# Kernel optimization log

Hardware: AMD Instinct MI355X
Metric: run time of the kernel (lower is better)

## Reference

```python
import jax, jax.numpy as jnp
import numpy as np

B, H, W, C = 128, 256, 1024, 1
N_HOLES = 5
PROB = 1.0
HOLE_MINW, HOLE_MAXW = W // 10, int(W / 2.5)   # 102, 409
HOLE_MINH, HOLE_MAXH = H // 10, int(H / 2.5)   # 25, 102


def setup_inputs() -> dict:
    key = jax.random.key(0)
    k0, k1, k2, k3, k4, k5 = jax.random.split(key, 6)
    x = jax.random.normal(k0, (B, H, W, C), dtype=jnp.float32)
    # hole centers: tf.random.uniform((bsz,n), 0, dim-1, int32) -> [0, dim-1)
    xs = jax.random.randint(k1, (B, N_HOLES), 0, W - 1, dtype=jnp.int32)
    ys = jax.random.randint(k2, (B, N_HOLES), 0, H - 1, dtype=jnp.int32)
    # hole sizes: raw in [0, max-min); reference adds the min offset
    xs_w_raw = jax.random.randint(k3, (B, N_HOLES), 0, HOLE_MAXW - HOLE_MINW, dtype=jnp.int32)
    ys_h_raw = jax.random.randint(k4, (B, N_HOLES), 0, HOLE_MAXH - HOLE_MINH, dtype=jnp.int32)
    # per-hole activation uniforms (hole active iff act_rand < PROB)
    act_rand = jax.random.uniform(k5, (B, N_HOLES), dtype=jnp.float32)
    return {"x": x, "xs": xs, "ys": ys, "xs_w_raw": xs_w_raw,
            "ys_h_raw": ys_h_raw, "act_rand": act_rand}


def _build_mask(xs, ys, xs_w_raw, ys_h_raw, act_rand):
    xs_w = xs_w_raw + HOLE_MINW                      # (B, N) hole widths
    ys_h = ys_h_raw + HOLE_MINH                      # (B, N) hole heights
    xs_start = jnp.clip(xs - xs_w // 2, 0, W - 2)
    xs_end   = jnp.clip(xs + xs_w // 2, 1, W - 1)
    ys_start = jnp.clip(ys - ys_h // 2, 0, H - 2)
    ys_end   = jnp.clip(ys + ys_h // 2, 1, H - 1)
    act = act_rand < PROB                            # (B, N) hole-wise activation
    idx_h = jnp.arange(H)
    idx_w = jnp.arange(W)
    mask = jnp.zeros((B, H, W), dtype=bool)
    for n in range(N_HOLES):                         # small fixed hole count
        mh = (ys_start[:, n, None] <= idx_h) & (idx_h <= ys_end[:, n, None])  # (B, H)
        mw = (xs_start[:, n, None] <= idx_w) & (idx_w <= xs_end[:, n, None])  # (B, W)
        m = mh[:, :, None] & mw[:, None, :]                                   # (B, H, W)
        mask = mask | (m & act[:, n, None, None])
    return mask


def reference(x, xs, ys, xs_w_raw, ys_h_raw, act_rand):
    mask = _build_mask(xs, ys, xs_w_raw, ys_h_raw, act_rand)   # (B, H, W) bool
    maskf = mask[..., None].astype(x.dtype)                    # (B, H, W, 1)
    fill = jnp.mean(x)  # hole_fill='min' path: hf = ones * reduce_mean(x)
    return x * (1.0 - maskf) + maskf * fill
```

## Files before the change

### kernel.cpp

```cpp
#include <hip/hip_runtime.h>


#define BB 128
#define HH 256
#define WW 1024
#define N_HOLES 5
#define HOLE_MINW (WW / 10)
#define HOLE_MINH (HH / 10)
#define N_ELEM (BB * HH * WW)
#define RED_BLOCKS 2048

__global__ __launch_bounds__(256) void reduce_kernel(
    const float* __restrict__ x, float* __restrict__ partials) {
  int tid = blockIdx.x * blockDim.x + threadIdx.x;
  int stride = gridDim.x * blockDim.x;
  const float4* x4 = (const float4*)x;
  const int n4 = N_ELEM / 4;
  float s = 0.0f;
  for (int i = tid; i < n4; i += stride) {
    float4 v = x4[i];
    s += (v.x + v.y) + (v.z + v.w);
  }
  #pragma unroll
  for (int off = 32; off > 0; off >>= 1) s += __shfl_down(s, off, 64);
  __shared__ float wsum[4];
  int lane = threadIdx.x & 63;
  int wave = threadIdx.x >> 6;
  if (lane == 0) wsum[wave] = s;
  __syncthreads();
  if (threadIdx.x == 0)
    partials[blockIdx.x] = (wsum[0] + wsum[1]) + (wsum[2] + wsum[3]);
}

__global__ __launch_bounds__(256) void finalize_kernel(
    const float* __restrict__ partials, float* __restrict__ mean_out) {
  float s = 0.0f;
  for (int i = threadIdx.x; i < RED_BLOCKS; i += 256) s += partials[i];
  #pragma unroll
  for (int off = 32; off > 0; off >>= 1) s += __shfl_down(s, off, 64);
  __shared__ float wsum[4];
  int lane = threadIdx.x & 63;
  int wave = threadIdx.x >> 6;
  if (lane == 0) wsum[wave] = s;
  __syncthreads();
  if (threadIdx.x == 0) {
    float t = (wsum[0] + wsum[1]) + (wsum[2] + wsum[3]);
    mean_out[0] = t * (1.0f / (float)N_ELEM);
  }
}

__global__ __launch_bounds__(256) void apply_kernel(
    const float* __restrict__ x,
    const int* __restrict__ xs, const int* __restrict__ ys,
    const int* __restrict__ xs_w_raw, const int* __restrict__ ys_h_raw,
    const float* __restrict__ act_rand,
    const float* __restrict__ mean_ptr,
    float* __restrict__ out) {
  int row = blockIdx.x;
  int b = row >> 8;
  int h = row & 255;

  float mean = mean_ptr[0];

  int lo[N_HOLES], hi[N_HOLES];
  #pragma unroll
  for (int n = 0; n < N_HOLES; ++n) {
    int base = b * N_HOLES + n;
    int cx = xs[base];
    int cy = ys[base];
    int hw = (xs_w_raw[base] + HOLE_MINW) >> 1;
    int hh = (ys_h_raw[base] + HOLE_MINH) >> 1;
    int ys_s = min(max(cy - hh, 0), HH - 2);
    int ys_e = min(max(cy + hh, 1), HH - 1);
    bool act = act_rand[base] < 1.0f;
    bool in_row = act && (ys_s <= h) && (h <= ys_e);
    int xs_s = min(max(cx - hw, 0), WW - 2);
    int xs_e = min(max(cx + hw, 1), WW - 1);
    lo[n] = in_row ? xs_s : 1;
    hi[n] = in_row ? xs_e : 0;
  }

  int w0 = (int)threadIdx.x * 4;
  long idx = (long)row * WW + w0;
  float4 v = *(const float4*)(x + idx);
  float r[4] = {v.x, v.y, v.z, v.w};
  #pragma unroll
  for (int j = 0; j < 4; ++j) {
    int w = w0 + j;
    bool m = false;
    #pragma unroll
    for (int n = 0; n < N_HOLES; ++n)
      m = m || ((lo[n] <= w) && (w <= hi[n]));
    if (m) r[j] = mean;
  }
  float4 o;
  o.x = r[0]; o.y = r[1]; o.z = r[2]; o.w = r[3];
  *(float4*)(out + idx) = o;
}

extern "C" void kernel_launch(void* const* d_in, const int* in_sizes, int n_in,
                              void* d_out, int out_size, void* d_ws, size_t ws_size,
                              hipStream_t stream) {
  const float* x        = (const float*)d_in[0];
  const int* xs         = (const int*)d_in[1];
  const int* ys         = (const int*)d_in[2];
  const int* xs_w_raw   = (const int*)d_in[3];
  const int* ys_h_raw   = (const int*)d_in[4];
  const float* act_rand = (const float*)d_in[5];
  float* out = (float*)d_out;

  float* partials = (float*)d_ws;
  float* mean_ptr = partials + RED_BLOCKS;

  reduce_kernel<<<RED_BLOCKS, 256, 0, stream>>>(x, partials);
  finalize_kernel<<<1, 256, 0, stream>>>(partials, mean_ptr);
  apply_kernel<<<BB * HH, 256, 0, stream>>>(x, xs, ys, xs_w_raw, ys_h_raw,
                                            act_rand, mean_ptr, out);
}
```

Before: 269.5 us.

## Fuse copy into reduction pass and fill only hole rectangles afterward

```diff
diff --git a/kernel.cpp b/kernel.cpp
--- a/kernel.cpp
+++ b/kernel.cpp
@@ -9,16 +9,20 @@
 #define HOLE_MINH (HH / 10)
 #define N_ELEM (BB * HH * WW)
 #define RED_BLOCKS 2048
+#define ROW_SLICES 8
 
-__global__ __launch_bounds__(256) void reduce_kernel(
-    const float* __restrict__ x, float* __restrict__ partials) {
+__global__ __launch_bounds__(256) void copy_reduce_kernel(
+    const float* __restrict__ x, float* __restrict__ out,
+    float* __restrict__ partials) {
   int tid = blockIdx.x * blockDim.x + threadIdx.x;
   int stride = gridDim.x * blockDim.x;
   const float4* x4 = (const float4*)x;
+  float4* out4 = (float4*)out;
   const int n4 = N_ELEM / 4;
   float s = 0.0f;
   for (int i = tid; i < n4; i += stride) {
     float4 v = x4[i];
+    out4[i] = v;
     s += (v.x + v.y) + (v.z + v.w);
   }
   #pragma unroll
@@ -32,70 +36,52 @@
     partials[blockIdx.x] = (wsum[0] + wsum[1]) + (wsum[2] + wsum[3]);
 }
 
-__global__ __launch_bounds__(256) void finalize_kernel(
-    const float* __restrict__ partials, float* __restrict__ mean_out) {
+__global__ __launch_bounds__(256) void fill_holes_kernel(
+    const int* __restrict__ xs, const int* __restrict__ ys,
+    const int* __restrict__ xs_w_raw, const int* __restrict__ ys_h_raw,
+    const float* __restrict__ act_rand,
+    const float* __restrict__ partials,
+    float* __restrict__ out) {
   float s = 0.0f;
   for (int i = threadIdx.x; i < RED_BLOCKS; i += 256) s += partials[i];
   #pragma unroll
   for (int off = 32; off > 0; off >>= 1) s += __shfl_down(s, off, 64);
   __shared__ float wsum[4];
+  __shared__ float mean_sh;
   int lane = threadIdx.x & 63;
   int wave = threadIdx.x >> 6;
   if (lane == 0) wsum[wave] = s;
   __syncthreads();
   if (threadIdx.x == 0) {
     float t = (wsum[0] + wsum[1]) + (wsum[2] + wsum[3]);
-    mean_out[0] = t * (1.0f / (float)N_ELEM);
+    mean_sh = t * (1.0f / (float)N_ELEM);
   }
-}
+  __syncthreads();
+  float mean = mean_sh;
 
-__global__ __launch_bounds__(256) void apply_kernel(
-    const float* __restrict__ x,
-    const int* __restrict__ xs, const int* __restrict__ ys,
-    const int* __restrict__ xs_w_raw, const int* __restrict__ ys_h_raw,
-    const float* __restrict__ act_rand,
-    const float* __restrict__ mean_ptr,
-    float* __restrict__ out) {
-  int row = blockIdx.x;
-  int b = row >> 8;
-  int h = row & 255;
+  int bid = blockIdx.x;
+  int b = bid / (N_HOLES * ROW_SLICES);
+  int rem = bid % (N_HOLES * ROW_SLICES);
+  int n = rem / ROW_SLICES;
+  int slice = rem % ROW_SLICES;
 
-  float mean = mean_ptr[0];
+  int base = b * N_HOLES + n;
+  if (!(act_rand[base] < 1.0f)) return;
+  int cx = xs[base];
+  int cy = ys[base];
+  int hw = (xs_w_raw[base] + HOLE_MINW) >> 1;
+  int hh = (ys_h_raw[base] + HOLE_MINH) >> 1;
+  int ys_s = min(max(cy - hh, 0), HH - 2);
+  int ys_e = min(max(cy + hh, 1), HH - 1);
+  int xs_s = min(max(cx - hw, 0), WW - 2);
+  int xs_e = min(max(cx + hw, 1), WW - 1);
 
-  int lo[N_HOLES], hi[N_HOLES];
-  #pragma unroll
-  for (int n = 0; n < N_HOLES; ++n) {
-    int base = b * N_HOLES + n;
-    int cx = xs[base];
-    int cy = ys[base];
-    int hw = (xs_w_raw[base] + HOLE_MINW) >> 1;
-    int hh = (ys_h_raw[base] + HOLE_MINH) >> 1;
-    int ys_s = min(max(cy - hh, 0), HH - 2);
-    int ys_e = min(max(cy + hh, 1), HH - 1);
-    bool act = act_rand[base] < 1.0f;
-    bool in_row = act && (ys_s <= h) && (h <= ys_e);
-    int xs_s = min(max(cx - hw, 0), WW - 2);
-    int xs_e = min(max(cx + hw, 1), WW - 1);
-    lo[n] = in_row ? xs_s : 1;
-    hi[n] = in_row ? xs_e : 0;
+  for (int h = ys_s + slice; h <= ys_e; h += ROW_SLICES) {
+    long rowbase = (long)(b * HH + h) * WW;
+    for (int w = xs_s + (int)threadIdx.x; w <= xs_e; w += 256) {
+      out[rowbase + w] = mean;
+    }
   }
-
-  int w0 = (int)threadIdx.x * 4;
-  long idx = (long)row * WW + w0;
-  float4 v = *(const float4*)(x + idx);
-  float r[4] = {v.x, v.y, v.z, v.w};
-  #pragma unroll
-  for (int j = 0; j < 4; ++j) {
-    int w = w0 + j;
-    bool m = false;
-    #pragma unroll
-    for (int n = 0; n < N_HOLES; ++n)
-      m = m || ((lo[n] <= w) && (w <= hi[n]));
-    if (m) r[j] = mean;
-  }
-  float4 o;
-  o.x = r[0]; o.y = r[1]; o.z = r[2]; o.w = r[3];
-  *(float4*)(out + idx) = o;
 }
 
 extern "C" void kernel_launch(void* const* d_in, const int* in_sizes, int n_in,
@@ -110,10 +96,8 @@
   float* out = (float*)d_out;
 
   float* partials = (float*)d_ws;
-  float* mean_ptr = partials + RED_BLOCKS;
 
-  reduce_kernel<<<RED_BLOCKS, 256, 0, stream>>>(x, partials);
-  finalize_kernel<<<1, 256, 0, stream>>>(partials, mean_ptr);
-  apply_kernel<<<BB * HH, 256, 0, stream>>>(x, xs, ys, xs_w_raw, ys_h_raw,
-                                            act_rand, mean_ptr, out);
+  copy_reduce_kernel<<<RED_BLOCKS, 256, 0, stream>>>(x, out, partials);
+  fill_holes_kernel<<<BB * N_HOLES * ROW_SLICES, 256, 0, stream>>>(
+      xs, ys, xs_w_raw, ys_h_raw, act_rand, partials, out);
 }
```

Result: no change. 264.9 us (-1.7%).
